# Kernel optimization log

Hardware: AMD Instinct MI355X
Metric: run time of the kernel (lower is better)

The kernel has to match this reference:

```python
import jax, jax.numpy as jnp
import numpy as np

B, S = 32768, 512
DISCOUNT_FACTOR = 0.99
AVERAGE_LAMBDA = 0.9
EPS = 1e-8


def setup_inputs() -> dict:
    key = jax.random.key(0)
    k1, k2, k3 = jax.random.split(key, 3)
    values = jax.random.normal(k1, (B, S + 1, 1), dtype=jnp.float32)
    rewards = jax.random.normal(k2, (B, S, 1), dtype=jnp.float32)
    # sparse episode terminations (0/1 float mask, as used multiplicatively)
    dones = (jax.random.uniform(k3, (B, S, 1)) < 0.01).astype(jnp.float32)
    # learned params: raw_* = atanh(target), so tanh(raw_*) recovers the init
    lam_init = jnp.linspace(AVERAGE_LAMBDA - 0.05, AVERAGE_LAMBDA + 0.05, S,
                            dtype=jnp.float32)  # mean == AVERAGE_LAMBDA
    raw_lambd = jnp.arctanh(lam_init)
    raw_gamma = jnp.arctanh(jnp.array([DISCOUNT_FACTOR], dtype=jnp.float32))
    return {"values": values, "rewards": rewards, "dones": dones,
            "raw_gamma": raw_gamma, "raw_lambd": raw_lambd}


def reference(values, rewards, dones, raw_gamma, raw_lambd):
    # GammaLambdaLearner.calculate_lambda_returns over the full seq_range
    gamma = jnp.maximum(jnp.tanh(raw_gamma), EPS)        # [1]
    lambdas = jnp.maximum(jnp.tanh(raw_lambd), EPS)      # [S]

    # time-major xs for the reversed scan
    v_next = jnp.swapaxes(values[:, 1:, :], 0, 1)        # [S, B, 1]
    r = jnp.swapaxes(rewards, 0, 1)                      # [S, B, 1]
    d = jnp.swapaxes(dones, 0, 1)                        # [S, B, 1]

    def step(ret_next, xs):
        lam, vt1, rt, dt = xs
        # bootstrap mix of next value and next lambda-return
        boot = (1.0 - lam) * vt1 + lam * ret_next
        ret = rt + gamma * (1.0 - dt) * boot
        return ret, ret

    init = values[:, -1, :]                              # [B, 1] terminal value
    _, rets = jax.lax.scan(step, init, (lambdas, v_next, r, d), reverse=True)
    return jnp.swapaxes(rets, 0, 1)                      # [B, S, 1]
```

## Files before the change

### kernel.cpp

```cpp
#include <hip/hip_runtime.h>

#define BATCH 32768
#define SEQ 512
#define TPL 8
#define EPS 1e-8f

__global__ void __launch_bounds__(256)
glr_wave_scan3(const float* __restrict__ values,
               const float* __restrict__ rewards,
               const float* __restrict__ dones,
               const float* __restrict__ raw_gamma,
               const float* __restrict__ raw_lambd,
               float* __restrict__ out) {
    const int lane = threadIdx.x & 63;
    const int wv   = threadIdx.x >> 6;
    const int row  = blockIdx.x * 4 + wv;
    const int t0   = lane * TPL;

    const float* __restrict__ vrow = values  + (size_t)row * (SEQ + 1);
    const float* __restrict__ rrow = rewards + (size_t)row * SEQ + t0;
    const float* __restrict__ drow = dones   + (size_t)row * SEQ + t0;
    float*       __restrict__ orow = out     + (size_t)row * SEQ + t0;

    float vj[TPL];
    #pragma unroll
    for (int j = 0; j < TPL; ++j)
        vj[j] = vrow[1 + t0 + j];

    const float4 r4a = *(const float4*)(rrow);
    const float4 r4b = *(const float4*)(rrow + 4);
    const float4 d4a = *(const float4*)(drow);
    const float4 d4b = *(const float4*)(drow + 4);
    const float4 l4a = *(const float4*)(raw_lambd + t0);
    const float4 l4b = *(const float4*)(raw_lambd + t0 + 4);
    const float vlast = vrow[SEQ];

    const float gamma = fmaxf(tanhf(raw_gamma[0]), EPS);

    float rj[TPL] = {r4a.x, r4a.y, r4a.z, r4a.w, r4b.x, r4b.y, r4b.z, r4b.w};
    float dj[TPL] = {d4a.x, d4a.y, d4a.z, d4a.w, d4b.x, d4b.y, d4b.z, d4b.w};
    const float lr[TPL] = {l4a.x, l4a.y, l4a.z, l4a.w, l4b.x, l4b.y, l4b.z, l4b.w};
    float lm[TPL];
    #pragma unroll
    for (int j = 0; j < TPL; ++j)
        lm[j] = fmaxf(tanhf(lr[j]), EPS);

    float a[TPL], b[TPL];
    float A = 1.f, Bv = 0.f;
    #pragma unroll
    for (int j = TPL - 1; j >= 0; --j) {
        const float g = gamma * (1.f - dj[j]);
        a[j] = g * lm[j];
        b[j] = fmaf(g * (1.f - lm[j]), vj[j], rj[j]);
        Bv = fmaf(a[j], Bv, b[j]);
        A  = a[j] * A;
    }

    #pragma unroll
    for (int dlt = 1; dlt < 64; dlt <<= 1) {
        const float oA = __shfl_down(A, dlt, 64);
        const float oB = __shfl_down(Bv, dlt, 64);
        if (lane + dlt < 64) {
            Bv = fmaf(A, oB, Bv);
            A  = A * oA;
        }
    }
    float EA = __shfl_down(A, 1, 64);
    float EB = __shfl_down(Bv, 1, 64);
    if (lane == 63) { EA = 1.f; EB = 0.f; }

    float ret = fmaf(EA, vlast, EB);

    float o[TPL];
    #pragma unroll
    for (int j = TPL - 1; j >= 0; --j) {
        ret = fmaf(a[j], ret, b[j]);
        o[j] = ret;
    }
    *(float4*)(orow)     = make_float4(o[0], o[1], o[2], o[3]);
    *(float4*)(orow + 4) = make_float4(o[4], o[5], o[6], o[7]);
}

extern "C" void kernel_launch(void* const* d_in, const int* in_sizes, int n_in,
                              void* d_out, int out_size, void* d_ws, size_t ws_size,
                              hipStream_t stream) {
    const float* values    = (const float*)d_in[0];
    const float* rewards   = (const float*)d_in[1];
    const float* dones     = (const float*)d_in[2];
    const float* raw_gamma = (const float*)d_in[3];
    const float* raw_lambd = (const float*)d_in[4];
    float* out = (float*)d_out;

    const int block = 256;
    const int grid = BATCH / 4;
    glr_wave_scan3<<<grid, block, 0, stream>>>(
        values, rewards, dones, raw_gamma, raw_lambd, out);
}
```

Before: 214.7 us.

## Process four rows per wave with double-buffered loads and hoisted lambda terms

Each wave now handles four rows instead of one. It prefetches the next row's values, rewards and dones into a second register buffer while scanning the current row. The tanh of lambda and gamma and their products are computed once per wave and reused across the rows. This is meant to hide global-load latency and amortize the per-row setup, at the cost of higher register pressure and a grid a quarter of the size.

```diff
diff --git a/kernel.cpp b/kernel.cpp
--- a/kernel.cpp
+++ b/kernel.cpp
@@ -4,54 +4,50 @@
 #define SEQ 512
 #define TPL 8
 #define EPS 1e-8f
+#define ROWS 4
 
-__global__ void __launch_bounds__(256)
-glr_wave_scan3(const float* __restrict__ values,
-               const float* __restrict__ rewards,
-               const float* __restrict__ dones,
-               const float* __restrict__ raw_gamma,
-               const float* __restrict__ raw_lambd,
-               float* __restrict__ out) {
-    const int lane = threadIdx.x & 63;
-    const int wv   = threadIdx.x >> 6;
-    const int row  = blockIdx.x * 4 + wv;
-    const int t0   = lane * TPL;
 
+struct RowBuf {
+    float  vj[TPL];
+    float4 ra, rb;
+    float4 da, db;
+    float  vlast;
+};
+
+__device__ __forceinline__ void load_row(const float* __restrict__ values,
+                                         const float* __restrict__ rewards,
+                                         const float* __restrict__ dones,
+                                         int row, int t0, RowBuf& b) {
     const float* __restrict__ vrow = values  + (size_t)row * (SEQ + 1);
     const float* __restrict__ rrow = rewards + (size_t)row * SEQ + t0;
     const float* __restrict__ drow = dones   + (size_t)row * SEQ + t0;
-    float*       __restrict__ orow = out     + (size_t)row * SEQ + t0;
-
-    float vj[TPL];
     #pragma unroll
     for (int j = 0; j < TPL; ++j)
-        vj[j] = vrow[1 + t0 + j];
+        b.vj[j] = vrow[1 + t0 + j];
+    b.ra = *(const float4*)(rrow);
+    b.rb = *(const float4*)(rrow + 4);
+    b.da = *(const float4*)(drow);
+    b.db = *(const float4*)(drow + 4);
+    b.vlast = vrow[SEQ];
+}
 
-    const float4 r4a = *(const float4*)(rrow);
-    const float4 r4b = *(const float4*)(rrow + 4);
-    const float4 d4a = *(const float4*)(drow);
-    const float4 d4b = *(const float4*)(drow + 4);
-    const float4 l4a = *(const float4*)(raw_lambd + t0);
-    const float4 l4b = *(const float4*)(raw_lambd + t0 + 4);
-    const float vlast = vrow[SEQ];
-
-    const float gamma = fmaxf(tanhf(raw_gamma[0]), EPS);
-
-    float rj[TPL] = {r4a.x, r4a.y, r4a.z, r4a.w, r4b.x, r4b.y, r4b.z, r4b.w};
-    float dj[TPL] = {d4a.x, d4a.y, d4a.z, d4a.w, d4b.x, d4b.y, d4b.z, d4b.w};
-    const float lr[TPL] = {l4a.x, l4a.y, l4a.z, l4a.w, l4b.x, l4b.y, l4b.z, l4b.w};
-    float lm[TPL];
-    #pragma unroll
-    for (int j = 0; j < TPL; ++j)
-        lm[j] = fmaxf(tanhf(lr[j]), EPS);
+__device__ __forceinline__ void compute_store(float* __restrict__ out,
+                                              int row, int t0, int lane,
+                                              const float gl[TPL],
+                                              const float gl1[TPL],
+                                              const RowBuf& bu) {
+    const float rj[TPL] = {bu.ra.x, bu.ra.y, bu.ra.z, bu.ra.w,
+                           bu.rb.x, bu.rb.y, bu.rb.z, bu.rb.w};
+    const float dj[TPL] = {bu.da.x, bu.da.y, bu.da.z, bu.da.w,
+                           bu.db.x, bu.db.y, bu.db.z, bu.db.w};
 
     float a[TPL], b[TPL];
     float A = 1.f, Bv = 0.f;
     #pragma unroll
     for (int j = TPL - 1; j >= 0; --j) {
-        const float g = gamma * (1.f - dj[j]);
-        a[j] = g * lm[j];
-        b[j] = fmaf(g * (1.f - lm[j]), vj[j], rj[j]);
+        const float e = 1.f - dj[j];
+        a[j] = gl[j] * e;
+        b[j] = fmaf(gl1[j] * e, bu.vj[j], rj[j]);
         Bv = fmaf(a[j], Bv, b[j]);
         A  = a[j] * A;
     }
@@ -69,7 +65,7 @@
     float EB = __shfl_down(Bv, 1, 64);
     if (lane == 63) { EA = 1.f; EB = 0.f; }
 
-    float ret = fmaf(EA, vlast, EB);
+    float ret = fmaf(EA, bu.vlast, EB);
 
     float o[TPL];
     #pragma unroll
@@ -77,8 +73,47 @@
         ret = fmaf(a[j], ret, b[j]);
         o[j] = ret;
     }
+    float* __restrict__ orow = out + (size_t)row * SEQ + t0;
     *(float4*)(orow)     = make_float4(o[0], o[1], o[2], o[3]);
     *(float4*)(orow + 4) = make_float4(o[4], o[5], o[6], o[7]);
+}
+
+__global__ void __launch_bounds__(256)
+glr_wave_scan4(const float* __restrict__ values,
+               const float* __restrict__ rewards,
+               const float* __restrict__ dones,
+               const float* __restrict__ raw_gamma,
+               const float* __restrict__ raw_lambd,
+               float* __restrict__ out) {
+    const int lane = threadIdx.x & 63;
+    const int wv   = threadIdx.x >> 6;
+    const int wave = blockIdx.x * 4 + wv;
+    const int row0 = wave * ROWS;
+    const int t0   = lane * TPL;
+
+    RowBuf A, B;
+    load_row(values, rewards, dones, row0 + 0, t0, A);
+
+    const float gamma = fmaxf(tanhf(raw_gamma[0]), EPS);
+    const float4 l4a = *(const float4*)(raw_lambd + t0);
+    const float4 l4b = *(const float4*)(raw_lambd + t0 + 4);
+    const float lr[TPL] = {l4a.x, l4a.y, l4a.z, l4a.w,
+                           l4b.x, l4b.y, l4b.z, l4b.w};
+    float gl[TPL], gl1[TPL];
+    #pragma unroll
+    for (int j = 0; j < TPL; ++j) {
+        const float lm = fmaxf(tanhf(lr[j]), EPS);
+        gl[j]  = gamma * lm;
+        gl1[j] = gamma * (1.f - lm);
+    }
+
+    load_row(values, rewards, dones, row0 + 1, t0, B);
+    compute_store(out, row0 + 0, t0, lane, gl, gl1, A);
+    load_row(values, rewards, dones, row0 + 2, t0, A);
+    compute_store(out, row0 + 1, t0, lane, gl, gl1, B);
+    load_row(values, rewards, dones, row0 + 3, t0, B);
+    compute_store(out, row0 + 2, t0, lane, gl, gl1, A);
+    compute_store(out, row0 + 3, t0, lane, gl, gl1, B);
 }
 
 extern "C" void kernel_launch(void* const* d_in, const int* in_sizes, int n_in,
@@ -92,7 +127,7 @@
     float* out = (float*)d_out;
 
     const int block = 256;
-    const int grid = BATCH / 4;
-    glr_wave_scan3<<<grid, block, 0, stream>>>(
+    const int grid  = BATCH / (4 * ROWS);
+    glr_wave_scan4<<<grid, block, 0, stream>>>(
         values, rewards, dones, raw_gamma, raw_lambd, out);
 }
```

Measured after the change: 225.6 us. 5.1% more time.
